# Kernel tuning notes

Hardware: AMD Instinct MI355X
Metric: run time of the kernel (lower is better)

Reference implementation:

```python
import jax, jax.numpy as jnp
import numpy as np

D_STATE = 16
D_CONV = 4


def rmsnorm(x, w, eps=1e-6):
    # normalize over last (channel) axis
    return x * jax.lax.rsqrt(jnp.mean(x * x, axis=-1, keepdims=True) + eps) * w


def silu(x):
    return x * jax.nn.sigmoid(x)


def mamba(x, in_proj_w, conv1d_w, conv1d_b, x_proj_w, dt_proj_w, dt_proj_b, A_log, D_param, out_proj_w):
    # x: [B, L, C], d_inner == C (expand=1)
    B, L, C = x.shape
    dt_rank = dt_proj_w.shape[1]
    xz = jnp.einsum('blc,ec->ble', x, in_proj_w)  # [B, L, 2C]
    u, z = jnp.split(xz, 2, axis=-1)
    # causal depthwise conv1d over time (pad left d_conv-1)
    uc = jax.lax.conv_general_dilated(
        u.transpose(0, 2, 1), conv1d_w[:, None, :], (1,), [(D_CONV - 1, 0)],
        dimension_numbers=('NCH', 'OIH', 'NCH'), feature_group_count=C)
    u = silu((uc + conv1d_b[None, :, None]).transpose(0, 2, 1))  # [B, L, C]
    x_dbl = jnp.einsum('blc,ec->ble', u, x_proj_w)  # [B, L, dt_rank + 2*N]
    dt, Bm, Cm = jnp.split(x_dbl, [dt_rank, dt_rank + D_STATE], axis=-1)
    delta = jax.nn.softplus(jnp.einsum('blr,dr->bld', dt, dt_proj_w) + dt_proj_b)  # [B, L, C]
    A = -jnp.exp(A_log)  # [C, N]
    deltaA = jnp.exp(delta[..., None] * A)              # [B, L, C, N]
    deltaBu = (delta * u)[..., None] * Bm[:, :, None, :]  # [B, L, C, N]

    def step(h, inp):
        dA, dBu, c = inp
        h = dA * h + dBu
        return h, jnp.einsum('bdn,bn->bd', h, c)

    h0 = jnp.zeros((B, C, D_STATE), x.dtype)
    _, ys = jax.lax.scan(step, h0, (deltaA.transpose(1, 0, 2, 3),
                                    deltaBu.transpose(1, 0, 2, 3),
                                    Cm.transpose(1, 0, 2)))
    y = ys.transpose(1, 0, 2) + u * D_param  # [B, L, C]
    y = y * silu(z)
    return jnp.einsum('bld,od->blo', y, out_proj_w)


def reference(x, norm_w, in_proj_w, conv1d_w, conv1d_b, x_proj_w, dt_proj_w, dt_proj_b,
              A_log, D_param, out_proj_w, scale_mod, dw_w, dw_b, res_scale):
    B, C, H, W = x.shape
    x_cl = x.transpose(0, 2, 3, 1)              # [B, H, W, C]
    xn_cl = rmsnorm(x_cl, norm_w)
    x_norm = xn_cl.transpose(0, 3, 1, 2)        # [B, C, H, W]
    # bidirectional Mamba over flattened spatial sequence
    x_flat = xn_cl.reshape(B, H * W, C)
    mparams = (in_proj_w, conv1d_w, conv1d_b, x_proj_w, dt_proj_w, dt_proj_b, A_log, D_param, out_proj_w)
    fwd = mamba(x_flat, *mparams)
    bwd = jnp.flip(mamba(jnp.flip(x_flat, axis=1), *mparams), axis=1)
    g = (fwd + bwd) * scale_mod
    global_feat = g.reshape(B, H, W, C).transpose(0, 3, 1, 2)
    # local spatial gating: sigmoid(depthwise 3x3 conv) * x_norm
    conv = jax.lax.conv_general_dilated(
        x_norm, dw_w[:, None, :, :], (1, 1), [(1, 1), (1, 1)],
        dimension_numbers=('NCHW', 'OIHW', 'NCHW'), feature_group_count=C)
    local_feat = jax.nn.sigmoid(conv + dw_b[None, :, None, None]) * x_norm
    return x + res_scale * (global_feat + local_feat)


def setup_inputs() -> dict:
    key = jax.random.key(0)
    ks = jax.random.split(key, 10)
    B, C, H, W = 8, 384, 32, 32
    dt_rank = 24  # ceil(384 / 16)
    s = 0.02
    f32 = jnp.float32
    return {
        'x': jax.random.normal(ks[0], (B, C, H, W), f32),
        'norm_w': jnp.ones((C,), f32),
        'in_proj_w': jax.random.normal(ks[1], (2 * C, C), f32) * s,
        'conv1d_w': jax.random.normal(ks[2], (C, D_CONV), f32) * 0.2,
        'conv1d_b': jnp.zeros((C,), f32),
        'x_proj_w': jax.random.normal(ks[3], (dt_rank + 2 * D_STATE, C), f32) * s,
        'dt_proj_w': jax.random.normal(ks[4], (C, dt_rank), f32) * 0.1,
        'dt_proj_b': jax.random.uniform(ks[5], (C,), f32, -4.0, -2.0),
        'A_log': jnp.log(jnp.tile(jnp.arange(1, D_STATE + 1, dtype=f32), (C, 1))),
        'D_param': jnp.ones((C,), f32),
        'out_proj_w': jax.random.normal(ks[6], (C, C), f32) * s,
        'scale_mod': jnp.full((1,), 0.25, f32),
        'dw_w': jax.random.normal(ks[7], (C, 3, 3), f32) * 0.1,
        'dw_b': jnp.zeros((C,), f32),
        'res_scale': jnp.full((1,), 0.5, f32),
    }
```

## Files before the change

kernel.cpp:

```cpp
#include <hip/hip_runtime.h>
#include <hip/hip_bf16.h>


typedef __attribute__((ext_vector_type(8))) short bf16x8;
typedef __attribute__((ext_vector_type(8))) unsigned short u16x8;
typedef __attribute__((ext_vector_type(4))) float f32x4;

#define L2E 1.44269504088896340736f

static __device__ __forceinline__ unsigned short f2bf(float f) {
  unsigned int u = __builtin_bit_cast(unsigned int, f);
  u += 0x7fff + ((u >> 16) & 1);
  return (unsigned short)(u >> 16);
}
static __device__ __forceinline__ float bf2f(unsigned short u) {
  unsigned int v = (unsigned int)u << 16;
  return __builtin_bit_cast(float, v);
}

__global__ __launch_bounds__(256) void prep_k(
    const float* __restrict__ in_w, const float* __restrict__ x_w,
    const float* __restrict__ dt_w, const float* __restrict__ out_w,
    const float* __restrict__ A_log, const float* __restrict__ nw,
    unsigned short* __restrict__ W_in, unsigned short* __restrict__ W_x,
    unsigned short* __restrict__ W_dt, unsigned short* __restrict__ W_out,
    float* __restrict__ A2) {
  int idx = blockIdx.x * 256 + threadIdx.x;
  switch (blockIdx.y) {
    case 0: if (idx < 768 * 384) W_in[idx] = f2bf(in_w[idx] * nw[idx % 384]); break;
    case 1: if (idx < 64 * 384) { int n = idx / 384, k = idx - n * 384;
              W_x[idx] = f2bf(n < 56 ? x_w[n * 384 + k] : 0.f); } break;
    case 2: if (idx < 384 * 32) { int n = idx >> 5, k = idx & 31;
              W_dt[idx] = f2bf(k < 24 ? dt_w[n * 24 + k] : 0.f); } break;
    case 3: if (idx < 384 * 384) W_out[idx] = f2bf(out_w[idx]); break;
    case 4: if (idx < 384 * 16) A2[idx] = -expf(A_log[idx]) * L2E; break;
  }
}

__global__ __launch_bounds__(256) void transpose_k(
    const float* __restrict__ x, unsigned short* __restrict__ xb,
    float* __restrict__ nf) {
  const int b = blockIdx.y;
  const int l0 = blockIdx.x * 32;
  const int tid = threadIdx.x;
  const int cr = tid >> 5, lw = tid & 31;
  const int cj = tid & 63, lr = tid >> 6;
  __shared__ float t64[64][33];
  __shared__ float part[8][33];
  float acc = 0.f;
  for (int cc = 0; cc < 6; ++cc) {
    #pragma unroll
    for (int k = 0; k < 8; ++k) {
      int cp = k * 8 + cr;
      int c = cc * 64 + cp;
      float v = x[(((size_t)(b * 384 + c)) << 10) + l0 + lw];
      t64[cp][lw] = v;
      acc = fmaf(v, v, acc);
    }
    __syncthreads();
    #pragma unroll
    for (int k2 = 0; k2 < 8; ++k2) {
      int ll = lr + 4 * k2;
      xb[((size_t)((b << 10) + l0 + ll)) * 384 + cc * 64 + cj] = f2bf(t64[cj][ll]);
    }
    __syncthreads();
  }
  part[cr][lw] = acc;
  __syncthreads();
  if (tid < 32) {
    float s = part[0][tid] + part[1][tid] + part[2][tid] + part[3][tid] +
              part[4][tid] + part[5][tid] + part[6][tid] + part[7][tid];
    nf[(b << 10) + l0 + tid] = rsqrtf(s * (1.f / 384.f) + 1e-6f);
  }
}

template <int EPI>
__global__ __launch_bounds__(256) void gemm_k(
    const unsigned short* __restrict__ A0u, const unsigned short* __restrict__ A1u,
    const unsigned short* __restrict__ Bw, int K, int N,
    float* __restrict__ of0, float* __restrict__ of1,
    unsigned short* __restrict__ ob0, unsigned short* __restrict__ ob1,
    const float* __restrict__ aux) {
  const unsigned short* A = blockIdx.z ? A1u : A0u;
  float* outf = blockIdx.z ? of1 : of0;
  unsigned short* outb = blockIdx.z ? ob1 : ob0;
  __shared__ unsigned short As[64][40];
  __shared__ unsigned short Bs[64][40];
  const int m0 = blockIdx.x * 64, n0 = blockIdx.y * 64;
  const int tid = threadIdx.x;
  const int lane = tid & 63, wave = tid >> 6;
  const int wm = wave >> 1, wn = wave & 1;
  const int lrow = tid >> 2, lseg = (tid & 3) * 8;
  const int fr = lane & 15, ks = (lane >> 4) * 8;
  f32x4 acc[2][2] = {};
  for (int k0 = 0; k0 < K; k0 += 32) {
    __syncthreads();
    *(bf16x8*)&As[lrow][lseg] = *(const bf16x8*)&A[(size_t)(m0 + lrow) * K + k0 + lseg];
    *(bf16x8*)&Bs[lrow][lseg] = *(const bf16x8*)&Bw[(size_t)(n0 + lrow) * K + k0 + lseg];
    __syncthreads();
    bf16x8 a0 = *(const bf16x8*)&As[wm * 32 + fr][ks];
    bf16x8 a1 = *(const bf16x8*)&As[wm * 32 + 16 + fr][ks];
    bf16x8 b0 = *(const bf16x8*)&Bs[wn * 32 + fr][ks];
    bf16x8 b1 = *(const bf16x8*)&Bs[wn * 32 + 16 + fr][ks];
    acc[0][0] = __builtin_amdgcn_mfma_f32_16x16x32_bf16(a0, b0, acc[0][0], 0, 0, 0);
    acc[0][1] = __builtin_amdgcn_mfma_f32_16x16x32_bf16(a0, b1, acc[0][1], 0, 0, 0);
    acc[1][0] = __builtin_amdgcn_mfma_f32_16x16x32_bf16(a1, b0, acc[1][0], 0, 0, 0);
    acc[1][1] = __builtin_amdgcn_mfma_f32_16x16x32_bf16(a1, b1, acc[1][1], 0, 0, 0);
  }
  #pragma unroll
  for (int mi = 0; mi < 2; ++mi)
    #pragma unroll
    for (int ni = 0; ni < 2; ++ni)
      #pragma unroll
      for (int j = 0; j < 4; ++j) {
        int m = m0 + wm * 32 + mi * 16 + (lane >> 4) * 4 + j;
        int n = n0 + wn * 32 + ni * 16 + (lane & 15);
        float v = acc[mi][ni][j];
        if (EPI == 0) {
          outb[(size_t)m * N + n] = f2bf(v * aux[m]);
        } else if (EPI == 1) {
          if (n < 24) outb[m * 32 + n] = f2bf(v);
          else if (n < 32) outb[m * 32 + n] = 0;
          if (n >= 24 && n < 56) outf[m * 32 + (n - 24)] = v;
        } else if (EPI == 2) {
          float t = v + aux[n];
          float sp = (t > 20.f) ? t : log1pf(expf(t));
          outb[(size_t)m * N + n] = f2bf(sp);
        } else {
          outf[(size_t)m * N + n] = v * aux[0];
        }
      }
}

__global__ __launch_bounds__(384) void conv_silu_k(
    const unsigned short* __restrict__ xz, const float* __restrict__ cw,
    const float* __restrict__ cb,
    unsigned short* __restrict__ ub0, unsigned short* __restrict__ ub1) {
  const int st = blockIdx.x, b = blockIdx.y, dir = blockIdx.z;
  const int c = threadIdx.x;
  const int s0 = st * 8;
  const float w0 = cw[c * 4 + 0], w1 = cw[c * 4 + 1];
  const float w2 = cw[c * 4 + 2], w3 = cw[c * 4 + 3];
  const float bb = cb[c];
  unsigned short* ub = dir ? ub1 : ub0;
  float xv[11];
  #pragma unroll
  for (int k = 0; k < 11; ++k) {
    int j = s0 - 3 + k;
    float v = 0.f;
    if (j >= 0) {
      int t = dir ? (1023 - j) : j;
      v = bf2f(xz[(size_t)((b << 10) + t) * 768 + c]);
    }
    xv[k] = v;
  }
  #pragma unroll
  for (int s = 0; s < 8; ++s) {
    float a = bb + xv[s] * w0 + xv[s + 1] * w1 + xv[s + 2] * w2 + xv[s + 3] * w3;
    float uv = a * __builtin_amdgcn_rcpf(1.f + __builtin_amdgcn_exp2f(-a * L2E));
    ub[(size_t)((b << 10) + s0 + s) * 384 + c] = f2bf(uv);
  }
}

__global__ __launch_bounds__(256) void scan1_k(
    const unsigned short* __restrict__ de0, const unsigned short* __restrict__ de1,
    const unsigned short* __restrict__ ub0, const unsigned short* __restrict__ ub1,
    const float* __restrict__ bc0, const float* __restrict__ bc1,
    const float* __restrict__ A2,
    float* __restrict__ Pseg, float* __restrict__ Hseg) {
  const int ct = blockIdx.x, b = blockIdx.y;
  const int dir = blockIdx.z >> 4, seg = blockIdx.z & 15;
  const unsigned short* del = dir ? de1 : de0;
  const unsigned short* uu  = dir ? ub1 : ub0;
  const float* bc  = dir ? bc1 : bc0;
  const int tid = threadIdx.x;
  const int lane = tid & 63, wave = tid >> 6;
  const int n = lane & 15, cg = lane >> 4;
  const int cl = wave * 4 + cg;
  const int c = ct * 16 + cl;
  const float a2 = A2[c * 16 + n];
  const size_t base = ((size_t)b << 10) + seg * 64;
  __shared__ __attribute__((aligned(16))) float sd[2][16][20];
  __shared__ __attribute__((aligned(16))) float sdu[2][16][20];
  __shared__ __attribute__((aligned(16))) float sB[2][16][20];
  const int li = tid >> 4, lj = tid & 15;
  unsigned short rd, ru; float rb;
  auto issue = [&](int s0) {
    size_t rowi = base + s0 + li;
    rd = del[rowi * 384 + ct * 16 + lj];
    ru = uu [rowi * 384 + ct * 16 + lj];
    rb = bc [rowi * 32 + lj];
  };
  auto commit = [&](int buf) {
    float dd = bf2f(rd), uv = bf2f(ru);
    sd[buf][lj][li] = dd; sdu[buf][lj][li] = dd * uv; sB[buf][lj][li] = rb;
  };
  issue(0); commit(0);
  float h = 0.f, P = 1.f;
  for (int ch = 0; ch < 4; ++ch) {
    const int cur = ch & 1;
    if (ch + 1 < 4) issue((ch + 1) * 16);
    __syncthreads();
    f32x4 dv[4], duv[4], bmv[4];
    #pragma unroll
    for (int r = 0; r < 4; ++r) {
      dv[r]  = *(const f32x4*)&sd[cur][cl][r * 4];
      duv[r] = *(const f32x4*)&sdu[cur][cl][r * 4];
      bmv[r] = *(const f32x4*)&sB[cur][n][r * 4];
    }
    #pragma unroll
    for (int i = 0; i < 16; ++i) {
      float dA = __builtin_amdgcn_exp2f(dv[i >> 2][i & 3] * a2);
      h = fmaf(dA, h, duv[i >> 2][i & 3] * bmv[i >> 2][i & 3]);
      P *= dA;
    }
    if (ch + 1 < 4) { __syncthreads(); commit(cur ^ 1); }
  }
  size_t o = (size_t)((dir * 8 + b) * 16 + seg) * 6144 + c * 16 + n;
  Pseg[o] = P; Hseg[o] = h;
}

__global__ __launch_bounds__(256) void scomb_k(
    const float* __restrict__ Pseg, const float* __restrict__ Hseg,
    float* __restrict__ Hin) {
  const int db = blockIdx.y;
  const int r = blockIdx.x * 256 + threadIdx.x;
  float h = 0.f;
  #pragma unroll
  for (int s = 0; s < 16; ++s) {
    size_t o = (size_t)(db * 16 + s) * 6144 + r;
    Hin[o] = h;
    h = Pseg[o] * h + Hseg[o];
  }
}

__global__ __launch_bounds__(256) void scan2_k(
    const unsigned short* __restrict__ de0, const unsigned short* __restrict__ de1,
    const unsigned short* __restrict__ ub0, const unsigned short* __restrict__ ub1,
    const float* __restrict__ bc0, const float* __restrict__ bc1,
    const unsigned short* __restrict__ xz, const float* __restrict__ A2,
    const float* __restrict__ Dp, const float* __restrict__ Hin,
    unsigned short* __restrict__ Sb0, unsigned short* __restrict__ Sb1) {
  const int ct = blockIdx.x, b = blockIdx.y;
  const int dir = blockIdx.z >> 4, seg = blockIdx.z & 15;
  const unsigned short* del = dir ? de1 : de0;
  const unsigned short* uu  = dir ? ub1 : ub0;
  const float* bc  = dir ? bc1 : bc0;
  unsigned short* S = dir ? Sb1 : Sb0;
  const int tid = threadIdx.x;
  const int lane = tid & 63, wave = tid >> 6;
  const int n = lane & 15, cg = lane >> 4;
  const int cl = wave * 4 + cg;
  const int c = ct * 16 + cl;
  const float a2 = A2[c * 16 + n];
  const float dpc = Dp[c];
  const size_t base = (size_t)b << 10;
  const int segoff = seg * 64;
  __shared__ __attribute__((aligned(16))) float sd[2][16][20];
  __shared__ __attribute__((aligned(16))) float sdu[2][16][20];
  __shared__ __attribute__((aligned(16))) float su[2][16][20];
  __shared__ __attribute__((aligned(16))) float sz[2][16][20];
  __shared__ __attribute__((aligned(16))) float sbc[2][32][20];
  const int li = tid >> 4, lj = tid & 15;
  const int bi = tid >> 5, bj = tid & 31;
  unsigned short rd, ru, rz; float rb0, rb1;
  auto issue = [&](int s0) {
    size_t rowi = base + segoff + s0 + li;
    rd = del[rowi * 384 + ct * 16 + lj];
    ru = uu [rowi * 384 + ct * 16 + lj];
    int t = dir ? (1023 - (segoff + s0 + li)) : (segoff + s0 + li);
    rz = xz[(base + t) * 768 + 384 + ct * 16 + lj];
    rb0 = bc[(base + segoff + s0 + bi) * 32 + bj];
    rb1 = bc[(base + segoff + s0 + bi + 8) * 32 + bj];
  };
  auto commit = [&](int buf) {
    float dd = bf2f(rd), uv = bf2f(ru);
    sd[buf][lj][li] = dd; sdu[buf][lj][li] = dd * uv;
    su[buf][lj][li] = uv; sz[buf][lj][li] = bf2f(rz);
    sbc[buf][bj][bi] = rb0; sbc[buf][bj][bi + 8] = rb1;
  };
  issue(0); commit(0);
  float h = Hin[(size_t)((dir * 8 + b) * 16 + seg) * 6144 + c * 16 + n];
  for (int ch = 0; ch < 4; ++ch) {
    const int cur = ch & 1;
    if (ch + 1 < 4) issue((ch + 1) * 16);
    __syncthreads();
    f32x4 dv[4], duv[4], bmv[4], cmv[4];
    #pragma unroll
    for (int r = 0; r < 4; ++r) {
      dv[r]  = *(const f32x4*)&sd[cur][cl][r * 4];
      duv[r] = *(const f32x4*)&sdu[cur][cl][r * 4];
      bmv[r] = *(const f32x4*)&sbc[cur][n][r * 4];
      cmv[r] = *(const f32x4*)&sbc[cur][16 + n][r * 4];
    }
    float p[16];
    #pragma unroll
    for (int i = 0; i < 16; ++i) {
      float dA = __builtin_amdgcn_exp2f(dv[i >> 2][i & 3] * a2);
      h = fmaf(dA, h, duv[i >> 2][i & 3] * bmv[i >> 2][i & 3]);
      p[i] = h * cmv[i >> 2][i & 3];
    }
    float q8[8];
    #pragma unroll
    for (int j = 0; j < 8; ++j) {
      float send = (n & 8) ? p[j] : p[j + 8];
      float recv = __shfl_xor(send, 8);
      float keep = (n & 8) ? p[j + 8] : p[j];
      q8[j] = keep + recv;
    }
    float q4[4];
    #pragma unroll
    for (int j = 0; j < 4; ++j) {
      float send = (n & 4) ? q8[j] : q8[j + 4];
      float recv = __shfl_xor(send, 4);
      float keep = (n & 4) ? q8[j + 4] : q8[j];
      q4[j] = keep + recv;
    }
    float q2[2];
    #pragma unroll
    for (int j = 0; j < 2; ++j) {
      float send = (n & 2) ? q4[j] : q4[j + 2];
      float recv = __shfl_xor(send, 2);
      float keep = (n & 2) ? q4[j + 2] : q4[j];
      q2[j] = keep + recv;
    }
    float send = (n & 1) ? q2[0] : q2[1];
    float recv = __shfl_xor(send, 1);
    float keep = (n & 1) ? q2[1] : q2[0];
    float ysum = keep + recv;
    float uvn = su[cur][cl][n];
    float zz  = sz[cur][cl][n];
    float sig = __builtin_amdgcn_rcpf(1.f + __builtin_amdgcn_exp2f(-zz * L2E));
    float y = (ysum + uvn * dpc) * (zz * sig);
    int s = segoff + ch * 16 + n;
    int t = dir ? (1023 - s) : s;
    S[(base + t) * 384 + c] = f2bf(y);
    if (ch + 1 < 4) { __syncthreads(); commit(cur ^ 1); }
  }
}

__global__ __launch_bounds__(256) void ssum_k(
    const unsigned short* __restrict__ S0, const unsigned short* __restrict__ S1,
    unsigned short* __restrict__ Sb) {
  int i = blockIdx.x * 256 + threadIdx.x;
  u16x8 a = ((const u16x8*)S0)[i];
  u16x8 b = ((const u16x8*)S1)[i];
  u16x8 r;
  #pragma unroll
  for (int j = 0; j < 8; ++j) r[j] = f2bf(bf2f(a[j]) + bf2f(b[j]));
  ((u16x8*)Sb)[i] = r;
}

__global__ __launch_bounds__(256) void final_k(
    const float* __restrict__ G, const unsigned short* __restrict__ xb,
    const float* __restrict__ nf, const float* __restrict__ nw,
    const float* __restrict__ x, const float* __restrict__ dww,
    const float* __restrict__ dwb, const float* __restrict__ rs,
    float* __restrict__ out) {
  __shared__ float tile[64][33];
  const int l0 = blockIdx.x * 32, c0 = blockIdx.y * 64, b = blockIdx.z;
  const int tid = threadIdx.x;
  {
    const int cj = tid & 63, li = tid >> 6;
    const int c = c0 + cj;
    float w[9];
    #pragma unroll
    for (int q = 0; q < 9; ++q) w[q] = dww[c * 9 + q];
    const float bb = dwb[c];
    const float nwc = nw[c];
    for (int p = 0; p < 8; ++p) {
      int l = l0 + p * 4 + li;
      int hh = l >> 5, ww = l & 31;
      float acc = bb;
      #pragma unroll
      for (int di = -1; di <= 1; ++di) {
        int h2 = hh + di; if (h2 < 0 || h2 > 31) continue;
        #pragma unroll
        for (int dj = -1; dj <= 1; ++dj) {
          int w2 = ww + dj; if (w2 < 0 || w2 > 31) continue;
          int lp = h2 * 32 + w2;
          float xnv = bf2f(xb[(size_t)((b << 10) + lp) * 384 + c]) *
                      nf[(b << 10) + lp] * nwc;
          acc += xnv * w[(di + 1) * 3 + dj + 1];
        }
      }
      size_t ri = (size_t)((b << 10) + l) * 384 + c;
      float xv = bf2f(xb[ri]) * nf[(b << 10) + l] * nwc;
      float F = G[ri] + xv / (1.f + expf(-acc));
      tile[cj][p * 4 + li] = F;
    }
  }
  __syncthreads();
  {
    const int lw = tid & 31, cr = tid >> 5;
    const float rsv = rs[0];
    for (int p = 0; p < 8; ++p) {
      int c = c0 + p * 8 + cr;
      size_t o = ((size_t)(b * 384 + c) << 10) + l0 + lw;
      out[o] = x[o] + rsv * tile[p * 8 + cr][lw];
    }
  }
}

extern "C" void kernel_launch(void* const* d_in, const int* in_sizes, int n_in,
                              void* d_out, int out_size, void* d_ws, size_t ws_size,
                              hipStream_t stream) {
  const float* x         = (const float*)d_in[0];
  const float* norm_w    = (const float*)d_in[1];
  const float* in_proj_w = (const float*)d_in[2];
  const float* conv1d_w  = (const float*)d_in[3];
  const float* conv1d_b  = (const float*)d_in[4];
  const float* x_proj_w  = (const float*)d_in[5];
  const float* dt_proj_w = (const float*)d_in[6];
  const float* dt_proj_b = (const float*)d_in[7];
  const float* A_log     = (const float*)d_in[8];
  const float* D_param   = (const float*)d_in[9];
  const float* out_proj_w= (const float*)d_in[10];
  const float* scale_mod = (const float*)d_in[11];
  const float* dw_w      = (const float*)d_in[12];
  const float* dw_b      = (const float*)d_in[13];
  const float* res_scale = (const float*)d_in[14];
  float* out = (float*)d_out;

  char* base = (char*)d_ws;
  size_t off = 0;
  auto alloc = [&](size_t bytes) {
    off = (off + 255) & ~(size_t)255;
    void* p = base + off;
    off += bytes;
    return p;
  };
  const size_t B_BLC = (size_t)8192 * 384 * 2;

  unsigned short* xb   = (unsigned short*)alloc(B_BLC);
  float*          nf   = (float*)alloc((size_t)8192 * 4);
  unsigned short* xz   = (unsigned short*)alloc((size_t)8192 * 768 * 2);
  unsigned short* u_b0 = (unsigned short*)alloc(B_BLC);
  unsigned short* u_b1 = (unsigned short*)alloc(B_BLC);
  unsigned short* dtp0 = (unsigned short*)alloc((size_t)8192 * 32 * 2);
  unsigned short* dtp1 = (unsigned short*)alloc((size_t)8192 * 32 * 2);
  float*          bc0  = (float*)alloc((size_t)8192 * 32 * 4);
  float*          bc1  = (float*)alloc((size_t)8192 * 32 * 4);
  unsigned short* de0  = (unsigned short*)alloc(B_BLC);
  unsigned short* de1  = (unsigned short*)alloc(B_BLC);
  unsigned short* Sb0  = (unsigned short*)alloc(B_BLC);
  unsigned short* Sb1  = (unsigned short*)alloc(B_BLC);
  float*          Pseg = (float*)alloc((size_t)1572864 * 4);
  float*          Hseg = (float*)alloc((size_t)1572864 * 4);
  float*          Hin  = (float*)alloc((size_t)1572864 * 4);
  unsigned short* W_in = (unsigned short*)alloc((size_t)768 * 384 * 2);
  unsigned short* W_x  = (unsigned short*)alloc((size_t)64 * 384 * 2);
  unsigned short* W_dt = (unsigned short*)alloc((size_t)384 * 32 * 2);
  unsigned short* W_out= (unsigned short*)alloc((size_t)384 * 384 * 2);
  float*          A2   = (float*)alloc((size_t)384 * 16 * 4);
  float*          G    = (float*)alloc((size_t)8192 * 384 * 4);
  unsigned short* Ssum = de0;

  prep_k<<<dim3(1152, 5), 256, 0, stream>>>(in_proj_w, x_proj_w, dt_proj_w,
                                            out_proj_w, A_log, norm_w,
                                            W_in, W_x, W_dt, W_out, A2);
  transpose_k<<<dim3(32, 8), 256, 0, stream>>>(x, xb, nf);
  gemm_k<0><<<dim3(128, 12), 256, 0, stream>>>(xb, xb, W_in, 384, 768,
                                               nullptr, nullptr, xz, xz, nf);
  conv_silu_k<<<dim3(128, 8, 2), 384, 0, stream>>>(xz, conv1d_w, conv1d_b,
                                                   u_b0, u_b1);
  gemm_k<1><<<dim3(128, 1, 2), 256, 0, stream>>>(u_b0, u_b1, W_x, 384, 64,
                                                 bc0, bc1, dtp0, dtp1, nullptr);
  gemm_k<2><<<dim3(128, 6, 2), 256, 0, stream>>>(dtp0, dtp1, W_dt, 32, 384,
                                                 nullptr, nullptr, de0, de1,
                                                 dt_proj_b);
  scan1_k<<<dim3(24, 8, 32), 256, 0, stream>>>(de0, de1, u_b0, u_b1, bc0, bc1,
                                               A2, Pseg, Hseg);
  scomb_k<<<dim3(24, 16), 256, 0, stream>>>(Pseg, Hseg, Hin);
  scan2_k<<<dim3(24, 8, 32), 256, 0, stream>>>(de0, de1, u_b0, u_b1, bc0, bc1,
                                               xz, A2, D_param, Hin, Sb0, Sb1);
  ssum_k<<<1536, 256, 0, stream>>>(Sb0, Sb1, Ssum);
  gemm_k<3><<<dim3(128, 6), 256, 0, stream>>>(Ssum, Ssum, W_out, 384, 384,
                                              G, G, nullptr, nullptr, scale_mod);
  final_k<<<dim3(32, 6, 8), 256, 0, stream>>>(G, xb, nf, norm_w, x, dw_w, dw_b,
                                              res_scale, out);
}
```

Baseline: 263.6 us.

## Fuse bidirectional sum into out-proj GEMM, widen scan blocks, vectorize final kernel

The separate ssum kernel is removed. The two scan-direction outputs are now summed in bf16 while the out-projection GEMM loads its A tile, which drops one launch and one full read/write pass. The GEMM grid is swapped so that N tiles vary fastest, letting consecutive blocks share A rows in cache. Both scan kernels now handle 32 channels per 512-thread block instead of 16 per 256, and the final depthwise-conv kernel is rewritten to use 8-wide vector loads with weights premultiplied and cached in LDS, plus a fast sigmoid.

After: 257.8 us. 1.02x faster.

```diff
diff --git a/kernel.cpp b/kernel.cpp
--- a/kernel.cpp
+++ b/kernel.cpp
@@ -74,7 +74,7 @@
   }
 }
 
-template <int EPI>
+template <int EPI, int SUMIN>
 __global__ __launch_bounds__(256) void gemm_k(
     const unsigned short* __restrict__ A0u, const unsigned short* __restrict__ A1u,
     const unsigned short* __restrict__ Bw, int K, int N,
@@ -86,7 +86,7 @@
   unsigned short* outb = blockIdx.z ? ob1 : ob0;
   __shared__ unsigned short As[64][40];
   __shared__ unsigned short Bs[64][40];
-  const int m0 = blockIdx.x * 64, n0 = blockIdx.y * 64;
+  const int n0 = blockIdx.x * 64, m0 = blockIdx.y * 64;
   const int tid = threadIdx.x;
   const int lane = tid & 63, wave = tid >> 6;
   const int wm = wave >> 1, wn = wave & 1;
@@ -95,7 +95,16 @@
   f32x4 acc[2][2] = {};
   for (int k0 = 0; k0 < K; k0 += 32) {
     __syncthreads();
-    *(bf16x8*)&As[lrow][lseg] = *(const bf16x8*)&A[(size_t)(m0 + lrow) * K + k0 + lseg];
+    if (SUMIN) {
+      u16x8 va = *(const u16x8*)&A0u[(size_t)(m0 + lrow) * K + k0 + lseg];
+      u16x8 vb = *(const u16x8*)&A1u[(size_t)(m0 + lrow) * K + k0 + lseg];
+      u16x8 s;
+      #pragma unroll
+      for (int j = 0; j < 8; ++j) s[j] = f2bf(bf2f(va[j]) + bf2f(vb[j]));
+      *(u16x8*)&As[lrow][lseg] = s;
+    } else {
+      *(bf16x8*)&As[lrow][lseg] = *(const bf16x8*)&A[(size_t)(m0 + lrow) * K + k0 + lseg];
+    }
     *(bf16x8*)&Bs[lrow][lseg] = *(const bf16x8*)&Bw[(size_t)(n0 + lrow) * K + k0 + lseg];
     __syncthreads();
     bf16x8 a0 = *(const bf16x8*)&As[wm * 32 + fr][ks];
@@ -117,7 +126,7 @@
         int n = n0 + wn * 32 + ni * 16 + (lane & 15);
         float v = acc[mi][ni][j];
         if (EPI == 0) {
-          outb[(size_t)m * N + n] = f2bf(v * aux[m]);
+          ob0[(size_t)m * N + n] = f2bf(v * aux[m]);
         } else if (EPI == 1) {
           if (n < 24) outb[m * 32 + n] = f2bf(v);
           else if (n < 32) outb[m * 32 + n] = 0;
@@ -127,7 +136,7 @@
           float sp = (t > 20.f) ? t : log1pf(expf(t));
           outb[(size_t)m * N + n] = f2bf(sp);
         } else {
-          outf[(size_t)m * N + n] = v * aux[0];
+          of0[(size_t)m * N + n] = v * aux[0];
         }
       }
 }
@@ -162,7 +171,7 @@
   }
 }
 
-__global__ __launch_bounds__(256) void scan1_k(
+__global__ __launch_bounds__(512) void scan1_k(
     const unsigned short* __restrict__ de0, const unsigned short* __restrict__ de1,
     const unsigned short* __restrict__ ub0, const unsigned short* __restrict__ ub1,
     const float* __restrict__ bc0, const float* __restrict__ bc1,
@@ -177,18 +186,18 @@
   const int lane = tid & 63, wave = tid >> 6;
   const int n = lane & 15, cg = lane >> 4;
   const int cl = wave * 4 + cg;
-  const int c = ct * 16 + cl;
+  const int c = ct * 32 + cl;
   const float a2 = A2[c * 16 + n];
   const size_t base = ((size_t)b << 10) + seg * 64;
-  __shared__ __attribute__((aligned(16))) float sd[2][16][20];
-  __shared__ __attribute__((aligned(16))) float sdu[2][16][20];
-  __shared__ __attribute__((aligned(16))) float sB[2][16][20];
-  const int li = tid >> 4, lj = tid & 15;
+  __shared__ __attribute__((aligned(16))) float sd[2][32][20];
+  __shared__ __attribute__((aligned(16))) float sdu[2][32][20];
+  __shared__ __attribute__((aligned(16))) float sB[2][32][20];
+  const int li = tid >> 5, lj = tid & 31;
   unsigned short rd, ru; float rb;
   auto issue = [&](int s0) {
     size_t rowi = base + s0 + li;
-    rd = del[rowi * 384 + ct * 16 + lj];
-    ru = uu [rowi * 384 + ct * 16 + lj];
+    rd = del[rowi * 384 + ct * 32 + lj];
+    ru = uu [rowi * 384 + ct * 32 + lj];
     rb = bc [rowi * 32 + lj];
   };
   auto commit = [&](int buf) {
@@ -234,7 +243,7 @@
   }
 }
 
-__global__ __launch_bounds__(256) void scan2_k(
+__global__ __launch_bounds__(512) void scan2_k(
     const unsigned short* __restrict__ de0, const unsigned short* __restrict__ de1,
     const unsigned short* __restrict__ ub0, const unsigned short* __restrict__ ub1,
     const float* __restrict__ bc0, const float* __restrict__ bc1,
@@ -251,33 +260,31 @@
   const int lane = tid & 63, wave = tid >> 6;
   const int n = lane & 15, cg = lane >> 4;
   const int cl = wave * 4 + cg;
-  const int c = ct * 16 + cl;
+  const int c = ct * 32 + cl;
   const float a2 = A2[c * 16 + n];
   const float dpc = Dp[c];
   const size_t base = (size_t)b << 10;
   const int segoff = seg * 64;
-  __shared__ __attribute__((aligned(16))) float sd[2][16][20];
-  __shared__ __attribute__((aligned(16))) float sdu[2][16][20];
-  __shared__ __attribute__((aligned(16))) float su[2][16][20];
-  __shared__ __attribute__((aligned(16))) float sz[2][16][20];
+  __shared__ __attribute__((aligned(16))) float sd[2][32][20];
+  __shared__ __attribute__((aligned(16))) float sdu[2][32][20];
+  __shared__ __attribute__((aligned(16))) float su[2][32][20];
+  __shared__ __attribute__((aligned(16))) float sz[2][32][20];
   __shared__ __attribute__((aligned(16))) float sbc[2][32][20];
-  const int li = tid >> 4, lj = tid & 15;
-  const int bi = tid >> 5, bj = tid & 31;
-  unsigned short rd, ru, rz; float rb0, rb1;
+  const int li = tid >> 5, lj = tid & 31;
+  unsigned short rd, ru, rz; float rb;
   auto issue = [&](int s0) {
     size_t rowi = base + segoff + s0 + li;
-    rd = del[rowi * 384 + ct * 16 + lj];
-    ru = uu [rowi * 384 + ct * 16 + lj];
+    rd = del[rowi * 384 + ct * 32 + lj];
+    ru = uu [rowi * 384 + ct * 32 + lj];
     int t = dir ? (1023 - (segoff + s0 + li)) : (segoff + s0 + li);
-    rz = xz[(base + t) * 768 + 384 + ct * 16 + lj];
-    rb0 = bc[(base + segoff + s0 + bi) * 32 + bj];
-    rb1 = bc[(base + segoff + s0 + bi + 8) * 32 + bj];
+    rz = xz[(base + t) * 768 + 384 + ct * 32 + lj];
+    rb = bc[rowi * 32 + lj];
   };
   auto commit = [&](int buf) {
     float dd = bf2f(rd), uv = bf2f(ru);
     sd[buf][lj][li] = dd; sdu[buf][lj][li] = dd * uv;
     su[buf][lj][li] = uv; sz[buf][lj][li] = bf2f(rz);
-    sbc[buf][bj][bi] = rb0; sbc[buf][bj][bi + 8] = rb1;
+    sbc[buf][lj][li] = rb;
   };
   issue(0); commit(0);
   float h = Hin[(size_t)((dir * 8 + b) * 16 + seg) * 6144 + c * 16 + n];
@@ -339,18 +346,6 @@
   }
 }
 
-__global__ __launch_bounds__(256) void ssum_k(
-    const unsigned short* __restrict__ S0, const unsigned short* __restrict__ S1,
-    unsigned short* __restrict__ Sb) {
-  int i = blockIdx.x * 256 + threadIdx.x;
-  u16x8 a = ((const u16x8*)S0)[i];
-  u16x8 b = ((const u16x8*)S1)[i];
-  u16x8 r;
-  #pragma unroll
-  for (int j = 0; j < 8; ++j) r[j] = f2bf(bf2f(a[j]) + bf2f(b[j]));
-  ((u16x8*)Sb)[i] = r;
-}
-
 __global__ __launch_bounds__(256) void final_k(
     const float* __restrict__ G, const unsigned short* __restrict__ xb,
     const float* __restrict__ nf, const float* __restrict__ nw,
@@ -358,36 +353,59 @@
     const float* __restrict__ dwb, const float* __restrict__ rs,
     float* __restrict__ out) {
   __shared__ float tile[64][33];
+  __shared__ float wq[9][64];
+  __shared__ float bbs[64], nws[64];
   const int l0 = blockIdx.x * 32, c0 = blockIdx.y * 64, b = blockIdx.z;
   const int tid = threadIdx.x;
+  for (int i = tid; i < 576; i += 256) {
+    int c = i / 9, q = i - c * 9;
+    wq[q][c] = dww[(size_t)(c0 + c) * 9 + q] * nw[c0 + c];
+  }
+  if (tid < 64) { bbs[tid] = dwb[c0 + tid]; nws[tid] = nw[c0 + tid]; }
+  __syncthreads();
   {
-    const int cj = tid & 63, li = tid >> 6;
-    const int c = c0 + cj;
-    float w[9];
-    #pragma unroll
-    for (int q = 0; q < 9; ++q) w[q] = dww[c * 9 + q];
-    const float bb = dwb[c];
-    const float nwc = nw[c];
-    for (int p = 0; p < 8; ++p) {
-      int l = l0 + p * 4 + li;
-      int hh = l >> 5, ww = l & 31;
-      float acc = bb;
+    const int oct = tid & 7, li = tid >> 3;
+    const int l = l0 + li;
+    const int hh = l >> 5, ww = l & 31;
+    float acc[8];
+    {
+      f32x4 ba = *(const f32x4*)&bbs[oct * 8];
+      f32x4 bb2 = *(const f32x4*)&bbs[oct * 8 + 4];
       #pragma unroll
-      for (int di = -1; di <= 1; ++di) {
-        int h2 = hh + di; if (h2 < 0 || h2 > 31) continue;
+      for (int j = 0; j < 4; ++j) { acc[j] = ba[j]; acc[j + 4] = bb2[j]; }
+    }
+    #pragma unroll
+    for (int di = -1; di <= 1; ++di) {
+      int h2 = hh + di;
+      if (h2 < 0 || h2 > 31) continue;
+      #pragma unroll
+      for (int dj = -1; dj <= 1; ++dj) {
+        int w2 = ww + dj;
+        if (w2 < 0 || w2 > 31) continue;
+        int lp = h2 * 32 + w2;
+        float nfl = nf[(b << 10) + lp];
+        u16x8 v = *(const u16x8*)&xb[(size_t)((b << 10) + lp) * 384 + c0 + oct * 8];
+        int q = (di + 1) * 3 + (dj + 1);
+        f32x4 wa = *(const f32x4*)&wq[q][oct * 8];
+        f32x4 wb = *(const f32x4*)&wq[q][oct * 8 + 4];
         #pragma unroll
-        for (int dj = -1; dj <= 1; ++dj) {
-          int w2 = ww + dj; if (w2 < 0 || w2 > 31) continue;
-          int lp = h2 * 32 + w2;
-          float xnv = bf2f(xb[(size_t)((b << 10) + lp) * 384 + c]) *
-                      nf[(b << 10) + lp] * nwc;
-          acc += xnv * w[(di + 1) * 3 + dj + 1];
+        for (int j = 0; j < 4; ++j) {
+          acc[j]     = fmaf(bf2f(v[j]) * nfl, wa[j], acc[j]);
+          acc[j + 4] = fmaf(bf2f(v[j + 4]) * nfl, wb[j], acc[j + 4]);
         }
       }
-      size_t ri = (size_t)((b << 10) + l) * 384 + c;
-      float xv = bf2f(xb[ri]) * nf[(b << 10) + l] * nwc;
-      float F = G[ri] + xv / (1.f + expf(-acc));
-      tile[cj][p * 4 + li] = F;
+    }
+    size_t ri = (size_t)((b << 10) + l) * 384 + c0 + oct * 8;
+    float nfl0 = nf[(b << 10) + l];
+    u16x8 xc = *(const u16x8*)&xb[ri];
+    f32x4 g0 = *(const f32x4*)&G[ri];
+    f32x4 g1 = *(const f32x4*)&G[ri + 4];
+    #pragma unroll
+    for (int j = 0; j < 8; ++j) {
+      float xv = bf2f(xc[j]) * nfl0 * nws[oct * 8 + j];
+      float sig = __builtin_amdgcn_rcpf(1.f + __builtin_amdgcn_exp2f(-acc[j] * L2E));
+      float gg = (j < 4) ? g0[j] : g1[j - 4];
+      tile[oct * 8 + j][li] = gg + xv * sig;
     }
   }
   __syncthreads();
@@ -454,29 +472,28 @@
   unsigned short* W_out= (unsigned short*)alloc((size_t)384 * 384 * 2);
   float*          A2   = (float*)alloc((size_t)384 * 16 * 4);
   float*          G    = (float*)alloc((size_t)8192 * 384 * 4);
-  unsigned short* Ssum = de0;
 
   prep_k<<<dim3(1152, 5), 256, 0, stream>>>(in_proj_w, x_proj_w, dt_proj_w,
                                             out_proj_w, A_log, norm_w,
                                             W_in, W_x, W_dt, W_out, A2);
   transpose_k<<<dim3(32, 8), 256, 0, stream>>>(x, xb, nf);
-  gemm_k<0><<<dim3(128, 12), 256, 0, stream>>>(xb, xb, W_in, 384, 768,
-                                               nullptr, nullptr, xz, xz, nf);
+  gemm_k<0, 0><<<dim3(12, 128), 256, 0, stream>>>(xb, xb, W_in, 384, 768,
+                                                  nullptr, nullptr, xz, xz, nf);
   conv_silu_k<<<dim3(128, 8, 2), 384, 0, stream>>>(xz, conv1d_w, conv1d_b,
                                                    u_b0, u_b1);
-  gemm_k<1><<<dim3(128, 1, 2), 256, 0, stream>>>(u_b0, u_b1, W_x, 384, 64,
-                                                 bc0, bc1, dtp0, dtp1, nullptr);
-  gemm_k<2><<<dim3(128, 6, 2), 256, 0, stream>>>(dtp0, dtp1, W_dt, 32, 384,
-                                                 nullptr, nullptr, de0, de1,
-                                                 dt_proj_b);
-  scan1_k<<<dim3(24, 8, 32), 256, 0, stream>>>(de0, de1, u_b0, u_b1, bc0, bc1,
+  gemm_k<1, 0><<<dim3(1, 128, 2), 256, 0, stream>>>(u_b0, u_b1, W_x, 384, 64,
+                                                    bc0, bc1, dtp0, dtp1, nullptr);
+  gemm_k<2, 0><<<dim3(6, 128, 2), 256, 0, stream>>>(dtp0, dtp1, W_dt, 32, 384,
+                                                    nullptr, nullptr, de0, de1,
+                                                    dt_proj_b);
+  scan1_k<<<dim3(12, 8, 32), 512, 0, stream>>>(de0, de1, u_b0, u_b1, bc0, bc1,
                                                A2, Pseg, Hseg);
   scomb_k<<<dim3(24, 16), 256, 0, stream>>>(Pseg, Hseg, Hin);
-  scan2_k<<<dim3(24, 8, 32), 256, 0, stream>>>(de0, de1, u_b0, u_b1, bc0, bc1,
+  scan2_k<<<dim3(12, 8, 32), 512, 0, stream>>>(de0, de1, u_b0, u_b1, bc0, bc1,
                                                xz, A2, D_param, Hin, Sb0, Sb1);
-  ssum_k<<<1536, 256, 0, stream>>>(Sb0, Sb1, Ssum);
-  gemm_k<3><<<dim3(128, 6), 256, 0, stream>>>(Ssum, Ssum, W_out, 384, 384,
-                                              G, G, nullptr, nullptr, scale_mod);
+  gemm_k<3, 1><<<dim3(6, 128), 256, 0, stream>>>(Sb0, Sb1, W_out, 384, 384,
+                                                 G, G, nullptr, nullptr,
+                                                 scale_mod);
   final_k<<<dim3(32, 6, 8), 256, 0, stream>>>(G, xb, nf, norm_w, x, dw_w, dw_b,
                                               res_scale, out);
 }
```
